# Kernel tuning notes

Measured on AMD Instinct MI355X. Metric: run time of the kernel, lower is better.

The kernel has to match this reference:

```python
import jax, jax.numpy as jnp
import numpy as np

E, K, D, H = 8, 2, 1024, 2048   # num_experts, top_k, dim, ffn_dim
B, S = 1, 1024                   # batch, seq


def setup_inputs() -> dict:
    key = jax.random.key(0)
    k0, k1, k2, k3, k4 = jax.random.split(key, 5)
    sD = 1.0 / np.sqrt(D)
    sH = 1.0 / np.sqrt(H)
    return {
        "hidden_states": jax.random.normal(k0, (B, S, D), jnp.float32),
        "gate_w": jax.random.normal(k1, (E, D), jnp.float32) * sD,
        "w1": jax.random.normal(k2, (E, D, H), jnp.float32) * sD,
        "w2": jax.random.normal(k3, (E, H, D), jnp.float32) * sH,
        "w3": jax.random.normal(k4, (E, D, H), jnp.float32) * sD,
    }


def _grouped_swiglu(x_sorted, counts, w1, w2, w3):
    """Grouped expert SwiGLU over tokens sorted by expert id.

    x_sorted: [T, D] tokens grouped contiguously by expert (expert 0 first).
    counts:   [E] number of tokens per expert (sums to T).
    """
    if hasattr(jax.lax, "ragged_dot"):
        gs = counts.astype(jnp.int32)
        h = jax.nn.silu(jax.lax.ragged_dot(x_sorted, w1, gs)) * jax.lax.ragged_dot(x_sorted, w3, gs)
        return jax.lax.ragged_dot(h, w2, gs)
    # Fallback: per-expert masked GEMM (same math; zeros pass through silu*mul).
    pos = jnp.arange(x_sorted.shape[0])
    eid = jnp.searchsorted(jnp.cumsum(counts), pos, side="right")  # expert of each sorted token
    out = jnp.zeros((x_sorted.shape[0], w2.shape[-1]), x_sorted.dtype)
    for e in range(w1.shape[0]):
        xm = jnp.where((eid == e)[:, None], x_sorted, 0.0)
        he = jax.nn.silu(xm @ w1[e]) * (xm @ w3[e])
        out = out + he @ w2[e]
    return out


def reference(hidden_states, gate_w, w1, w2, w3):
    x = hidden_states.reshape(-1, D)                      # [N, D]
    N = x.shape[0]
    # --- router: softmax over experts, then top-k ---
    scores = jax.nn.softmax(x @ gate_w.T, axis=-1)        # [N, E]
    top_scores, sel = jax.lax.top_k(scores, K)            # [N, K]
    # flatten slot-major so flat_idx % N == token id (matches `% num_tokens`)
    sel_flat = sel.T.reshape(-1)                          # [K*N]
    scores_flat = top_scores.T.reshape(-1)                # [K*N]
    # --- reorder: stable sort by expert id ---
    order = jnp.argsort(sel_flat, stable=True)            # [K*N]
    tok_sorted = order % N                                # original token per routed slot
    scores_sorted = scores_flat[order]
    counts = jnp.bincount(sel_flat, length=E)             # tokens per expert
    # --- dispatch (ep_size=1: all-to-all is identity) + grouped expert GEMM ---
    x_sorted = x[tok_sorted]                              # [K*N, D]
    y = _grouped_swiglu(x_sorted, counts, w1, w2, w3)     # [K*N, D]
    # --- weighted scatter-combine ---
    weighted = y * scores_sorted[:, None]
    out = jnp.zeros((N, D), x.dtype).at[tok_sorted].add(weighted)
    return out.reshape(hidden_states.shape)
```

## Files before the change

### kernel.cpp

```cpp
#include <hip/hip_runtime.h>
#include <hip/hip_bf16.h>
#include <math.h>

#define NE 8
#define DD 1024
#define HH 2048
#define NTOK 1024
#define NSLOT 2048
#define NSLOTP 3072

typedef short short8v __attribute__((ext_vector_type(8)));
typedef float f32x4 __attribute__((ext_vector_type(4)));

static __device__ __forceinline__ unsigned short f2bf(float f) {
  union { __hip_bfloat16 h; unsigned short u; } c;
  c.h = __float2bfloat16(f);
  return c.u;
}

static __device__ __forceinline__ short8v pk8(const float* q) {
  short8v v;
#pragma unroll
  for (int i = 0; i < 8; ++i) v[i] = (short)f2bf(q[i]);
  return v;
}

static __device__ __forceinline__ void barrier_lds() {
  asm volatile("s_waitcnt lgkmcnt(0)" ::: "memory");
  __builtin_amdgcn_s_barrier();
  asm volatile("" ::: "memory");
}

__global__ __launch_bounds__(64) void krouter(const float* __restrict__ x,
                                              const float* __restrict__ gw,
                                              int* __restrict__ e_sel,
                                              float* __restrict__ w_sel) {
  int n = blockIdx.x;
  int lane = threadIdx.x;
  const float4* xr = (const float4*)(x + (size_t)n * DD);
  const float4* gr = (const float4*)gw;
  float acc[NE];
#pragma unroll
  for (int e = 0; e < NE; ++e) acc[e] = 0.f;
#pragma unroll
  for (int i = 0; i < 4; ++i) {
    float4 xv = xr[lane + i * 64];
#pragma unroll
    for (int e = 0; e < NE; ++e) {
      float4 gv = gr[e * 256 + lane + i * 64];
      acc[e] += xv.x * gv.x + xv.y * gv.y + xv.z * gv.z + xv.w * gv.w;
    }
  }
#pragma unroll
  for (int e = 0; e < NE; ++e)
#pragma unroll
    for (int off = 32; off > 0; off >>= 1) acc[e] += __shfl_xor(acc[e], off);
  if (lane == 0) {
    float m = acc[0];
#pragma unroll
    for (int e = 1; e < NE; ++e) m = fmaxf(m, acc[e]);
    float p[NE];
    float z = 0.f;
#pragma unroll
    for (int e = 0; e < NE; ++e) { p[e] = expf(acc[e] - m); z += p[e]; }
    float inv = 1.f / z;
    int e1 = 0;
#pragma unroll
    for (int e = 1; e < NE; ++e) if (acc[e] > acc[e1]) e1 = e;
    int e2 = (e1 == 0) ? 1 : 0;
#pragma unroll
    for (int e = 0; e < NE; ++e) if (e != e1 && acc[e] > acc[e2]) e2 = e;
    e_sel[n] = e1;         w_sel[n] = p[e1] * inv;
    e_sel[NTOK + n] = e2;  w_sel[NTOK + n] = p[e2] * inv;
  }
}

__global__ __launch_bounds__(256) void kbuild(const int* __restrict__ e_sel,
                                              const float* __restrict__ w_sel,
                                              int* __restrict__ tok,
                                              float* __restrict__ wgt,
                                              int* __restrict__ meta) {
  __shared__ int sc[NE], scur[NE];
  int t = threadIdx.x;
  if (t < NE) sc[t] = 0;
  __syncthreads();
  for (int s = t; s < NSLOTP; s += 256) tok[s] = -1;
  for (int s = t; s < NSLOT; s += 256) atomicAdd(&sc[e_sel[s]], 1);
  __syncthreads();
  if (t == 0) {
    int run = 0, i64 = 0, i128 = 0;
    for (int e = 0; e < NE; ++e) {
      meta[8 + e] = run; scur[e] = run;
      meta[e] = sc[e];
      int nm = (sc[e] + 127) >> 7;
      for (int m = 0; m < nm; ++m) {
        meta[128 + i128] = e; meta[152 + i128] = m; ++i128;
      }
      for (int m = 0; m < 2 * nm; ++m) {
        meta[32 + i64] = e; meta[80 + i64] = m; ++i64;
      }
      run += nm << 7;
    }
    meta[16] = i64; meta[17] = i128;
  }
  __syncthreads();
  for (int s = t; s < NSLOT; s += 256) {
    int e = e_sel[s];
    int pos = atomicAdd(&scur[e], 1);
    tok[pos] = s & (NTOK - 1);
    wgt[pos] = w_sel[s];
  }
}

__global__ __launch_bounds__(256) void kgather(const float* __restrict__ x,
                                               const int* __restrict__ tok,
                                               unsigned short* __restrict__ xg) {
  int tid = threadIdx.x;
  int row = blockIdx.x * 2 + (tid >> 7);
  int g = tid & 127;
  int t = tok[row];
  char* dst = (char*)xg + (size_t)row * 2048 + (g << 4);
  short8v v = {0, 0, 0, 0, 0, 0, 0, 0};
  if (t >= 0) {
    const float* src = x + (size_t)t * DD + g * 8;
    float q[8];
#pragma unroll
    for (int i = 0; i < 8; ++i) q[i] = src[i];
    v = pk8(q);
  }
  *(short8v*)dst = v;
}

__global__ __launch_bounds__(256, 2) void kgemm13(
    const unsigned short* __restrict__ xg, const float* __restrict__ w1,
    const float* __restrict__ w3, unsigned short* __restrict__ hws,
    const int* __restrict__ meta) {
  __shared__ __align__(16) char smem[32768];
  char* ldsA = smem;
  char* ldsB = smem + 16384;
  int vt = blockIdx.y;
  if (vt >= meta[17]) return;
  int e = meta[128 + vt], mt = meta[152 + vt];
  int n0 = blockIdx.x * 64;
  int abase = meta[8 + e] + mt * 128;
  int tid = threadIdx.x, l = tid & 63, w = tid >> 6;
  int wm = w & 1, wn = w >> 1;

  int arow = tid >> 2, ag = tid & 3;
  const char* paA = (const char*)xg + (size_t)(abase + arow) * 2048 + (ag << 4);
  int wbA = arow * 64 + (((ag ^ (arow >> 1)) & 3) << 4);
  int bn = tid & 63, kb = tid >> 6;
  const float* pb1 = w1 + (size_t)e * DD * HH + (size_t)(kb * 8) * HH + n0 + bn;
  const float* pb3 = w3 + (size_t)e * DD * HH + (size_t)(kb * 8) * HH + n0 + bn;
  int wbB = bn * 64 + (((kb ^ (bn >> 1)) & 3) << 4);

  int afo[4];
#pragma unroll
  for (int mf = 0; mf < 4; ++mf) {
    int r = wm * 64 + mf * 16 + (l & 15);
    afo[mf] = r * 64 + ((((l >> 4) ^ (r >> 1)) & 3) << 4);
  }
  int bfo[2];
#pragma unroll
  for (int nf = 0; nf < 2; ++nf) {
    int n = wn * 32 + nf * 16 + (l & 15);
    bfo[nf] = n * 64 + ((((l >> 4) ^ (n >> 1)) & 3) << 4);
  }

  f32x4 accg[4][2], accu[4][2];
#pragma unroll
  for (int i = 0; i < 4; ++i)
#pragma unroll
    for (int j = 0; j < 2; ++j) {
      accg[i][j] = (f32x4){0.f, 0.f, 0.f, 0.f};
      accu[i][j] = (f32x4){0.f, 0.f, 0.f, 0.f};
    }

  float q1A[8], q3A[8], q1B[8], q3B[8];
  short8v aqA[2], aqB[2];
  aqA[0] = *(const short8v*)(paA);
  aqA[1] = *(const short8v*)(paA + 131072);
#pragma unroll
  for (int j = 0; j < 8; ++j) {
    q1A[j] = pb1[(size_t)j * HH];
    q3A[j] = pb3[(size_t)j * HH];
  }
  *(short8v*)(ldsA + wbA) = aqA[0];
  *(short8v*)(ldsA + 4096 + wbA) = aqA[1];
  *(short8v*)(ldsB + wbB) = pk8(q1A);
  *(short8v*)(ldsB + 4096 + wbB) = pk8(q3A);
  aqB[0] = *(const short8v*)(paA + 64);
  aqB[1] = *(const short8v*)(paA + 131072 + 64);
#pragma unroll
  for (int j = 0; j < 8; ++j) {
    q1B[j] = pb1[(size_t)(32 + j) * HH];
    q3B[j] = pb3[(size_t)(32 + j) * HH];
  }
  barrier_lds();

#define STEP13(S, QW1, QW3, AQW, QN1, QN3, AQN)                                \
  {                                                                            \
    int bo = ((S) & 1) * 8192;                                                 \
    short8v af[4], b1f[2], b3f[2];                                             \
    _Pragma("unroll") for (int mf = 0; mf < 4; ++mf)                           \
        af[mf] = *(const short8v*)(ldsA + bo + afo[mf]);                       \
    _Pragma("unroll") for (int nf = 0; nf < 2; ++nf) {                         \
      b1f[nf] = *(const short8v*)(ldsB + bo + bfo[nf]);                        \
      b3f[nf] = *(const short8v*)(ldsB + bo + 4096 + bfo[nf]);                 \
    }                                                                          \
    if ((S) < 31) {                                                            \
      int wo = (((S) + 1) & 1) * 8192;                                         \
      *(short8v*)(ldsA + wo + wbA) = AQW[0];                                   \
      *(short8v*)(ldsA + wo + 4096 + wbA) = AQW[1];                            \
      *(short8v*)(ldsB + wo + wbB) = pk8(QW1);                                 \
      *(short8v*)(ldsB + wo + 4096 + wbB) = pk8(QW3);                          \
    }                                                                          \
    if ((S) < 30) {                                                            \
      AQN[0] = *(const short8v*)(paA + ((S) + 2) * 64);                        \
      AQN[1] = *(const short8v*)(paA + 131072 + ((S) + 2) * 64);               \
      size_t ko = (size_t)((S) + 2) * 32 * HH;                                 \
      _Pragma("unroll") for (int j = 0; j < 8; ++j) {                          \
        QN1[j] = pb1[ko + (size_t)j * HH];                                     \
        QN3[j] = pb3[ko + (size_t)j * HH];                                     \
      }                                                                        \
    }                                                                          \
    _Pragma("unroll") for (int nf = 0; nf < 2; ++nf)                           \
        _Pragma("unroll") for (int mf = 0; mf < 4; ++mf) {                     \
      accg[mf][nf] = __builtin_amdgcn_mfma_f32_16x16x32_bf16(                  \
          af[mf], b1f[nf], accg[mf][nf], 0, 0, 0);                             \
      accu[mf][nf] = __builtin_amdgcn_mfma_f32_16x16x32_bf16(                  \
          af[mf], b3f[nf], accu[mf][nf], 0, 0, 0);                             \
    }                                                                          \
    if ((S) < 31) barrier_lds();                                               \
  }

  for (int ss = 0; ss < 16; ++ss) {
    int s0 = 2 * ss;
    STEP13(s0, q1B, q3B, aqB, q1A, q3A, aqA);
    STEP13(s0 + 1, q1A, q3A, aqA, q1B, q3B, aqB);
  }
#undef STEP13

  __syncthreads();
  unsigned short* hl = (unsigned short*)smem;
#pragma unroll
  for (int mf = 0; mf < 4; ++mf)
#pragma unroll
    for (int nf = 0; nf < 2; ++nf)
#pragma unroll
      for (int rr = 0; rr < 4; ++rr) {
        int row = wm * 64 + mf * 16 + ((l >> 4) << 2) + rr;
        int col = wn * 32 + nf * 16 + (l & 15);
        float gv = accg[mf][nf][rr], uv = accu[mf][nf][rr];
        hl[row * 64 + col] = f2bf((gv / (1.f + __expf(-gv))) * uv);
      }
  __syncthreads();
#pragma unroll
  for (int p = 0; p < 4; ++p) {
    int idx = p * 256 + tid;
    int row = idx >> 3, g = idx & 7;
    int dp = abase + row;
    *(short8v*)((char*)hws + (size_t)dp * 4096 + (size_t)n0 * 2 + (g << 4)) =
        *(const short8v*)((const char*)hl + row * 128 + (g << 4));
  }
}

__global__ __launch_bounds__(256, 3) void kgemm2(
    const unsigned short* __restrict__ hws, const float* __restrict__ w2,
    float* __restrict__ out, const int* __restrict__ tok,
    const float* __restrict__ wgt, const int* __restrict__ meta) {
  __shared__ __align__(16) char smem[24576];
  char* ldsA = smem;
  char* ldsB = smem + 16384;
  int vt = blockIdx.y;
  if (vt >= meta[17]) return;
  int e = meta[128 + vt], mt = meta[152 + vt];
  int n0 = blockIdx.x * 64;
  int kz = blockIdx.z;
  int mbase = meta[8 + e] + mt * 128;
  int rem = meta[e] - mt * 128;
  int tid = threadIdx.x, l = tid & 63, w = tid >> 6;
  int wm = w & 1, wn = w >> 1;

  int arow = tid >> 2, ag = tid & 3;
  const char* paA = (const char*)hws + (size_t)(mbase + arow) * 4096 +
                    kz * 2048 + (ag << 4);
  int wbA = arow * 64 + (((ag ^ (arow >> 1)) & 3) << 4);
  int bn = tid & 63, kb = tid >> 6;
  const float* pb = w2 + (size_t)e * HH * DD +
                    (size_t)(kz * 1024 + kb * 8) * DD + n0 + bn;
  int wbB = bn * 64 + (((kb ^ (bn >> 1)) & 3) << 4);

  int afo[4];
#pragma unroll
  for (int mf = 0; mf < 4; ++mf) {
    int r = wm * 64 + mf * 16 + (l & 15);
    afo[mf] = r * 64 + ((((l >> 4) ^ (r >> 1)) & 3) << 4);
  }
  int bfo[2];
#pragma unroll
  for (int nf = 0; nf < 2; ++nf) {
    int n = wn * 32 + nf * 16 + (l & 15);
    bfo[nf] = n * 64 + ((((l >> 4) ^ (n >> 1)) & 3) << 4);
  }

  f32x4 acc[4][2];
#pragma unroll
  for (int i = 0; i < 4; ++i)
#pragma unroll
    for (int j = 0; j < 2; ++j) acc[i][j] = (f32x4){0.f, 0.f, 0.f, 0.f};

  float qA[8], qB[8];
  short8v aqA[2], aqB[2];
  aqA[0] = *(const short8v*)(paA);
  aqA[1] = *(const short8v*)(paA + 262144);
#pragma unroll
  for (int j = 0; j < 8; ++j) qA[j] = pb[(size_t)j * DD];
  *(short8v*)(ldsA + wbA) = aqA[0];
  *(short8v*)(ldsA + 4096 + wbA) = aqA[1];
  *(short8v*)(ldsB + wbB) = pk8(qA);
  aqB[0] = *(const short8v*)(paA + 64);
  aqB[1] = *(const short8v*)(paA + 262144 + 64);
#pragma unroll
  for (int j = 0; j < 8; ++j) qB[j] = pb[(size_t)(32 + j) * DD];
  barrier_lds();

#define STEP2(S, QW, AQW, QN, AQN)                                             \
  {                                                                            \
    int bo = ((S) & 1) * 8192;                                                 \
    int bob = ((S) & 1) * 4096;                                                \
    short8v af[4], bf[2];                                                      \
    _Pragma("unroll") for (int mf = 0; mf < 4; ++mf)                           \
        af[mf] = *(const short8v*)(ldsA + bo + afo[mf]);                       \
    _Pragma("unroll") for (int nf = 0; nf < 2; ++nf)                           \
        bf[nf] = *(const short8v*)(ldsB + bob + bfo[nf]);                      \
    if ((S) < 31) {                                                            \
      int wo = (((S) + 1) & 1) * 8192;                                         \
      int wob = (((S) + 1) & 1) * 4096;                                        \
      *(short8v*)(ldsA + wo + wbA) = AQW[0];                                   \
      *(short8v*)(ldsA + wo + 4096 + wbA) = AQW[1];                            \
      *(short8v*)(ldsB + wob + wbB) = pk8(QW);                                 \
    }                                                                          \
    if ((S) < 30) {                                                            \
      AQN[0] = *(const short8v*)(paA + ((S) + 2) * 64);                        \
      AQN[1] = *(const short8v*)(paA + 262144 + ((S) + 2) * 64);               \
      size_t ko = (size_t)((S) + 2) * 32 * DD;                                 \
      _Pragma("unroll") for (int j = 0; j < 8; ++j)                            \
          QN[j] = pb[ko + (size_t)j * DD];                                     \
    }                                                                          \
    _Pragma("unroll") for (int nf = 0; nf < 2; ++nf)                           \
        _Pragma("unroll") for (int mf = 0; mf < 4; ++mf)                       \
            acc[mf][nf] = __builtin_amdgcn_mfma_f32_16x16x32_bf16(             \
                af[mf], bf[nf], acc[mf][nf], 0, 0, 0);                         \
    if ((S) < 31) barrier_lds();                                               \
  }

  for (int ss = 0; ss < 16; ++ss) {
    int s0 = 2 * ss;
    STEP2(s0, qB, aqB, qA, aqA);
    STEP2(s0 + 1, qA, aqA, qB, aqB);
  }
#undef STEP2

#pragma unroll
  for (int mf = 0; mf < 4; ++mf)
#pragma unroll
    for (int rr = 0; rr < 4; ++rr) {
      int row = wm * 64 + mf * 16 + ((l >> 4) << 2) + rr;
      if (row < rem) {
        int t = tok[mbase + row];
        float wt = wgt[mbase + row];
#pragma unroll
        for (int nf = 0; nf < 2; ++nf)
          atomicAdd(out + (size_t)t * DD + n0 + wn * 32 + nf * 16 + (l & 15),
                    wt * acc[mf][nf][rr]);
      }
    }
}

extern "C" void kernel_launch(void* const* d_in, const int* in_sizes, int n_in,
                              void* d_out, int out_size, void* d_ws, size_t ws_size,
                              hipStream_t stream) {
  const float* x  = (const float*)d_in[0];
  const float* gw = (const float*)d_in[1];
  const float* w1 = (const float*)d_in[2];
  const float* w2 = (const float*)d_in[3];
  const float* w3 = (const float*)d_in[4];
  float* out = (float*)d_out;
  char* ws = (char*)d_ws;
  const size_t MB = 1024 * 1024;
  if (ws_size < 24 * MB) return;

  unsigned short* xg  = (unsigned short*)(ws);
  unsigned short* hws = (unsigned short*)(ws + 6 * MB);
  char* mb = ws + 20 * MB;
  int*   e_sel  = (int*)mb;
  float* w_sel  = (float*)(mb + 8192);
  int*   tok    = (int*)(mb + 16384);
  float* wgt    = (float*)(mb + 16384 + 12288);
  int*   meta   = (int*)(mb + 16384 + 24576);

  hipMemsetAsync(out, 0, (size_t)out_size * sizeof(float), stream);
  krouter<<<dim3(NTOK), 64, 0, stream>>>(x, gw, e_sel, w_sel);
  kbuild<<<1, 256, 0, stream>>>(e_sel, w_sel, tok, wgt, meta);
  kgather<<<dim3(NSLOTP / 2), 256, 0, stream>>>(x, tok, xg);
  kgemm13<<<dim3(32, 24), 256, 0, stream>>>(xg, w1, w3, hws, meta);
  kgemm2<<<dim3(16, 24, 2), 256, 0, stream>>>(hws, w2, out, tok, wgt, meta);
}
```

Before: 108.7 us.

## Load A fragments directly from global to registers and double K-step to 64

The gate/up GEMM kernel no longer stages the bf16 activation tile through LDS. Each lane now loads its MFMA A-fragments straight from global memory into registers, double-buffered across steps. The K step per iteration grows from 32 to 64, which halves the number of barriers and iterations and uses a wider 128-byte-row swizzle for the B (weight) tile. This removes the LDS write/read traffic for A and half the synchronization, at the cost of more registers and A tiles that are no longer shared through LDS across the waves that reuse them.

Measured after the change: 130.0 us. 19.5% more time.

```diff
diff --git a/kernel.cpp b/kernel.cpp
--- a/kernel.cpp
+++ b/kernel.cpp
@@ -136,8 +136,7 @@
     const float* __restrict__ w3, unsigned short* __restrict__ hws,
     const int* __restrict__ meta) {
   __shared__ __align__(16) char smem[32768];
-  char* ldsA = smem;
-  char* ldsB = smem + 16384;
+  char* ldsB = smem;
   int vt = blockIdx.y;
   if (vt >= meta[17]) return;
   int e = meta[128 + vt], mt = meta[152 + vt];
@@ -146,26 +145,27 @@
   int tid = threadIdx.x, l = tid & 63, w = tid >> 6;
   int wm = w & 1, wn = w >> 1;
 
-  int arow = tid >> 2, ag = tid & 3;
-  const char* paA = (const char*)xg + (size_t)(abase + arow) * 2048 + (ag << 4);
-  int wbA = arow * 64 + (((ag ^ (arow >> 1)) & 3) << 4);
   int bn = tid & 63, kb = tid >> 6;
   const float* pb1 = w1 + (size_t)e * DD * HH + (size_t)(kb * 8) * HH + n0 + bn;
   const float* pb3 = w3 + (size_t)e * DD * HH + (size_t)(kb * 8) * HH + n0 + bn;
-  int wbB = bn * 64 + (((kb ^ (bn >> 1)) & 3) << 4);
-
-  int afo[4];
+  int wb1 = bn * 128 + (((kb ^ ((bn >> 1) & 7)) & 7) << 4);
+  int wb2 = bn * 128 + ((((kb + 4) ^ ((bn >> 1) & 7)) & 7) << 4);
+
+  const char* pa[4];
 #pragma unroll
   for (int mf = 0; mf < 4; ++mf) {
     int r = wm * 64 + mf * 16 + (l & 15);
-    afo[mf] = r * 64 + ((((l >> 4) ^ (r >> 1)) & 3) << 4);
-  }
-  int bfo[2];
-#pragma unroll
-  for (int nf = 0; nf < 2; ++nf) {
-    int n = wn * 32 + nf * 16 + (l & 15);
-    bfo[nf] = n * 64 + ((((l >> 4) ^ (n >> 1)) & 3) << 4);
-  }
+    pa[mf] = (const char*)xg + (size_t)(abase + r) * 2048 + ((l >> 4) << 4);
+  }
+  int bfo[2][2];
+#pragma unroll
+  for (int ks = 0; ks < 2; ++ks)
+#pragma unroll
+    for (int nf = 0; nf < 2; ++nf) {
+      int n = wn * 32 + nf * 16 + (l & 15);
+      int g = ks * 4 + (l >> 4);
+      bfo[ks][nf] = n * 128 + (((g ^ ((n >> 1) & 7)) & 7) << 4);
+    }
 
   f32x4 accg[4][2], accu[4][2];
 #pragma unroll
@@ -176,68 +176,78 @@
       accu[i][j] = (f32x4){0.f, 0.f, 0.f, 0.f};
     }
 
-  float q1A[8], q3A[8], q1B[8], q3B[8];
-  short8v aqA[2], aqB[2];
-  aqA[0] = *(const short8v*)(paA);
-  aqA[1] = *(const short8v*)(paA + 131072);
+  float q1A[16], q3A[16], q1B[16], q3B[16];
+  short8v aA[8], aB[8];
+#pragma unroll
+  for (int mf = 0; mf < 4; ++mf)
+#pragma unroll
+    for (int ks = 0; ks < 2; ++ks)
+      aA[mf * 2 + ks] = *(const short8v*)(pa[mf] + ks * 64);
 #pragma unroll
   for (int j = 0; j < 8; ++j) {
-    q1A[j] = pb1[(size_t)j * HH];
-    q3A[j] = pb3[(size_t)j * HH];
-  }
-  *(short8v*)(ldsA + wbA) = aqA[0];
-  *(short8v*)(ldsA + 4096 + wbA) = aqA[1];
-  *(short8v*)(ldsB + wbB) = pk8(q1A);
-  *(short8v*)(ldsB + 4096 + wbB) = pk8(q3A);
-  aqB[0] = *(const short8v*)(paA + 64);
-  aqB[1] = *(const short8v*)(paA + 131072 + 64);
-#pragma unroll
-  for (int j = 0; j < 8; ++j) {
-    q1B[j] = pb1[(size_t)(32 + j) * HH];
-    q3B[j] = pb3[(size_t)(32 + j) * HH];
+    q1A[j] = pb1[(size_t)j * HH];        q1A[8 + j] = pb1[(size_t)(32 + j) * HH];
+    q3A[j] = pb3[(size_t)j * HH];        q3A[8 + j] = pb3[(size_t)(32 + j) * HH];
+  }
+  *(short8v*)(ldsB + wb1) = pk8(q1A);
+  *(short8v*)(ldsB + wb2) = pk8(q1A + 8);
+  *(short8v*)(ldsB + 8192 + wb1) = pk8(q3A);
+  *(short8v*)(ldsB + 8192 + wb2) = pk8(q3A + 8);
+  {
+    size_t ko = (size_t)64 * HH;
+#pragma unroll
+    for (int j = 0; j < 8; ++j) {
+      q1B[j] = pb1[ko + (size_t)j * HH];  q1B[8 + j] = pb1[ko + (size_t)(32 + j) * HH];
+      q3B[j] = pb3[ko + (size_t)j * HH];  q3B[8 + j] = pb3[ko + (size_t)(32 + j) * HH];
+    }
   }
   barrier_lds();
 
-#define STEP13(S, QW1, QW3, AQW, QN1, QN3, AQN)                                \
+#define STEP13(S, QW1, QW3, QN1, QN3, AC, AN)                                  \
   {                                                                            \
-    int bo = ((S) & 1) * 8192;                                                 \
-    short8v af[4], b1f[2], b3f[2];                                             \
-    _Pragma("unroll") for (int mf = 0; mf < 4; ++mf)                           \
-        af[mf] = *(const short8v*)(ldsA + bo + afo[mf]);                       \
-    _Pragma("unroll") for (int nf = 0; nf < 2; ++nf) {                         \
-      b1f[nf] = *(const short8v*)(ldsB + bo + bfo[nf]);                        \
-      b3f[nf] = *(const short8v*)(ldsB + bo + 4096 + bfo[nf]);                 \
-    }                                                                          \
-    if ((S) < 31) {                                                            \
-      int wo = (((S) + 1) & 1) * 8192;                                         \
-      *(short8v*)(ldsA + wo + wbA) = AQW[0];                                   \
-      *(short8v*)(ldsA + wo + 4096 + wbA) = AQW[1];                            \
-      *(short8v*)(ldsB + wo + wbB) = pk8(QW1);                                 \
-      *(short8v*)(ldsB + wo + 4096 + wbB) = pk8(QW3);                          \
-    }                                                                          \
-    if ((S) < 30) {                                                            \
-      AQN[0] = *(const short8v*)(paA + ((S) + 2) * 64);                        \
-      AQN[1] = *(const short8v*)(paA + 131072 + ((S) + 2) * 64);               \
-      size_t ko = (size_t)((S) + 2) * 32 * HH;                                 \
+    int bo = ((S) & 1) * 16384;                                                \
+    short8v b1f[2][2], b3f[2][2];                                              \
+    _Pragma("unroll") for (int ks = 0; ks < 2; ++ks)                           \
+        _Pragma("unroll") for (int nf = 0; nf < 2; ++nf) {                     \
+      b1f[ks][nf] = *(const short8v*)(ldsB + bo + bfo[ks][nf]);                \
+      b3f[ks][nf] = *(const short8v*)(ldsB + bo + 8192 + bfo[ks][nf]);         \
+    }                                                                          \
+    if ((S) < 15) {                                                            \
+      int wo = (((S) + 1) & 1) * 16384;                                        \
+      *(short8v*)(ldsB + wo + wb1) = pk8(QW1);                                 \
+      *(short8v*)(ldsB + wo + wb2) = pk8(QW1 + 8);                             \
+      *(short8v*)(ldsB + wo + 8192 + wb1) = pk8(QW3);                          \
+      *(short8v*)(ldsB + wo + 8192 + wb2) = pk8(QW3 + 8);                      \
+    }                                                                          \
+    if ((S) < 14) {                                                            \
+      size_t ko = (size_t)((S) + 2) * 64 * HH;                                 \
       _Pragma("unroll") for (int j = 0; j < 8; ++j) {                          \
         QN1[j] = pb1[ko + (size_t)j * HH];                                     \
+        QN1[8 + j] = pb1[ko + (size_t)(32 + j) * HH];                          \
         QN3[j] = pb3[ko + (size_t)j * HH];                                     \
+        QN3[8 + j] = pb3[ko + (size_t)(32 + j) * HH];                          \
       }                                                                        \
     }                                                                          \
-    _Pragma("unroll") for (int nf = 0; nf < 2; ++nf)                           \
-        _Pragma("unroll") for (int mf = 0; mf < 4; ++mf) {                     \
+    if ((S) < 15) {                                                            \
+      _Pragma("unroll") for (int mf = 0; mf < 4; ++mf)                         \
+          _Pragma("unroll") for (int ks = 0; ks < 2; ++ks)                     \
+              AN[mf * 2 + ks] =                                                \
+                  *(const short8v*)(pa[mf] + ((S) + 1) * 128 + ks * 64);       \
+    }                                                                          \
+    _Pragma("unroll") for (int ks = 0; ks < 2; ++ks)                           \
+        _Pragma("unroll") for (int nf = 0; nf < 2; ++nf)                       \
+            _Pragma("unroll") for (int mf = 0; mf < 4; ++mf) {                 \
       accg[mf][nf] = __builtin_amdgcn_mfma_f32_16x16x32_bf16(                  \
-          af[mf], b1f[nf], accg[mf][nf], 0, 0, 0);                             \
+          AC[mf * 2 + ks], b1f[ks][nf], accg[mf][nf], 0, 0, 0);                \
       accu[mf][nf] = __builtin_amdgcn_mfma_f32_16x16x32_bf16(                  \
-          af[mf], b3f[nf], accu[mf][nf], 0, 0, 0);                             \
-    }                                                                          \
-    if ((S) < 31) barrier_lds();                                               \
-  }
-
-  for (int ss = 0; ss < 16; ++ss) {
+          AC[mf * 2 + ks], b3f[ks][nf], accu[mf][nf], 0, 0, 0);                \
+    }                                                                          \
+    if ((S) < 15) barrier_lds();                                               \
+  }
+
+  for (int ss = 0; ss < 8; ++ss) {
     int s0 = 2 * ss;
-    STEP13(s0, q1B, q3B, aqB, q1A, q3A, aqA);
-    STEP13(s0 + 1, q1A, q3A, aqA, q1B, q3B, aqB);
+    STEP13(s0, q1B, q3B, q1A, q3A, aA, aB);
+    STEP13(s0 + 1, q1A, q3A, q1B, q3B, aB, aA);
   }
 #undef STEP13
 
```

## Split fused gate/up GEMM into two kernels with SwiGLU in second epilogue

Applied to the files above, without the earlier changes.

The fused W1/W3 grouped GEMM is split into two kernels. The first computes the gate projection and stores it as bf16 in a new workspace buffer. The second computes the up projection and applies SiLU(gate)*up in its epilogue. Each kernel holds half the accumulators and half the LDS, so occupancy can rise from 2 to 3 blocks per CU. The cost is an extra launch, the A tile being read twice, an extra bf16 round-trip of the gate activations through global memory, and gate values rounded to bf16 before SiLU.

Result: slower. 122.9 us (+13.0%).

```diff
diff --git a/kernel.cpp b/kernel.cpp
--- a/kernel.cpp
+++ b/kernel.cpp
@@ -16,6 +16,12 @@
   union { __hip_bfloat16 h; unsigned short u; } c;
   c.h = __float2bfloat16(f);
   return c.u;
+}
+
+static __device__ __forceinline__ float bf2f(unsigned short u) {
+  union { unsigned int i; float f; } c;
+  c.i = (unsigned)u << 16;
+  return c.f;
 }
 
 static __device__ __forceinline__ short8v pk8(const float* q) {
@@ -131,11 +137,10 @@
   *(short8v*)dst = v;
 }
 
-__global__ __launch_bounds__(256, 2) void kgemm13(
+__global__ __launch_bounds__(256, 3) void kgemmG(
     const unsigned short* __restrict__ xg, const float* __restrict__ w1,
-    const float* __restrict__ w3, unsigned short* __restrict__ hws,
-    const int* __restrict__ meta) {
-  __shared__ __align__(16) char smem[32768];
+    unsigned short* __restrict__ g_ws, const int* __restrict__ meta) {
+  __shared__ __align__(16) char smem[24576];
   char* ldsA = smem;
   char* ldsB = smem + 16384;
   int vt = blockIdx.y;
@@ -150,8 +155,7 @@
   const char* paA = (const char*)xg + (size_t)(abase + arow) * 2048 + (ag << 4);
   int wbA = arow * 64 + (((ag ^ (arow >> 1)) & 3) << 4);
   int bn = tid & 63, kb = tid >> 6;
-  const float* pb1 = w1 + (size_t)e * DD * HH + (size_t)(kb * 8) * HH + n0 + bn;
-  const float* pb3 = w3 + (size_t)e * DD * HH + (size_t)(kb * 8) * HH + n0 + bn;
+  const float* pb = w1 + (size_t)e * DD * HH + (size_t)(kb * 8) * HH + n0 + bn;
   int wbB = bn * 64 + (((kb ^ (bn >> 1)) & 3) << 4);
 
   int afo[4];
@@ -167,79 +171,63 @@
     bfo[nf] = n * 64 + ((((l >> 4) ^ (n >> 1)) & 3) << 4);
   }
 
-  f32x4 accg[4][2], accu[4][2];
+  f32x4 acc[4][2];
 #pragma unroll
   for (int i = 0; i < 4; ++i)
 #pragma unroll
-    for (int j = 0; j < 2; ++j) {
-      accg[i][j] = (f32x4){0.f, 0.f, 0.f, 0.f};
-      accu[i][j] = (f32x4){0.f, 0.f, 0.f, 0.f};
-    }
-
-  float q1A[8], q3A[8], q1B[8], q3B[8];
+    for (int j = 0; j < 2; ++j) acc[i][j] = (f32x4){0.f, 0.f, 0.f, 0.f};
+
+  float qA[8], qB[8];
   short8v aqA[2], aqB[2];
   aqA[0] = *(const short8v*)(paA);
   aqA[1] = *(const short8v*)(paA + 131072);
 #pragma unroll
-  for (int j = 0; j < 8; ++j) {
-    q1A[j] = pb1[(size_t)j * HH];
-    q3A[j] = pb3[(size_t)j * HH];
-  }
+  for (int j = 0; j < 8; ++j) qA[j] = pb[(size_t)j * HH];
   *(short8v*)(ldsA + wbA) = aqA[0];
   *(short8v*)(ldsA + 4096 + wbA) = aqA[1];
-  *(short8v*)(ldsB + wbB) = pk8(q1A);
-  *(short8v*)(ldsB + 4096 + wbB) = pk8(q3A);
+  *(short8v*)(ldsB + wbB) = pk8(qA);
   aqB[0] = *(const short8v*)(paA + 64);
   aqB[1] = *(const short8v*)(paA + 131072 + 64);
 #pragma unroll
-  for (int j = 0; j < 8; ++j) {
-    q1B[j] = pb1[(size_t)(32 + j) * HH];
-    q3B[j] = pb3[(size_t)(32 + j) * HH];
-  }
+  for (int j = 0; j < 8; ++j) qB[j] = pb[(size_t)(32 + j) * HH];
   barrier_lds();
 
-#define STEP13(S, QW1, QW3, AQW, QN1, QN3, AQN)                                \
+#define STEPG(S, QW, AQW, QN, AQN)                                             \
   {                                                                            \
     int bo = ((S) & 1) * 8192;                                                 \
-    short8v af[4], b1f[2], b3f[2];                                             \
+    int bob = ((S) & 1) * 4096;                                                \
+    short8v af[4], bf[2];                                                      \
     _Pragma("unroll") for (int mf = 0; mf < 4; ++mf)                           \
         af[mf] = *(const short8v*)(ldsA + bo + afo[mf]);                       \
-    _Pragma("unroll") for (int nf = 0; nf < 2; ++nf) {                         \
-      b1f[nf] = *(const short8v*)(ldsB + bo + bfo[nf]);                        \
-      b3f[nf] = *(const short8v*)(ldsB + bo + 4096 + bfo[nf]);                 \
-    }                                                                          \
+    _Pragma("unroll") for (int nf = 0; nf < 2; ++nf)                           \
+        bf[nf] = *(const short8v*)(ldsB + bob + bfo[nf]);                      \
     if ((S) < 31) {                                                            \
       int wo = (((S) + 1) & 1) * 8192;                                         \
+      int wob = (((S) + 1) & 1) * 4096;                                        \
       *(short8v*)(ldsA + wo + wbA) = AQW[0];                                   \
       *(short8v*)(ldsA + wo + 4096 + wbA) = AQW[1];                            \
-      *(short8v*)(ldsB + wo + wbB) = pk8(QW1);                                 \
-      *(short8v*)(ldsB + wo + 4096 + wbB) = pk8(QW3);                          \
+      *(short8v*)(ldsB + wob + wbB) = pk8(QW);                                 \
     }                                                                          \
     if ((S) < 30) {                                                            \
       AQN[0] = *(const short8v*)(paA + ((S) + 2) * 64);                        \
       AQN[1] = *(const short8v*)(paA + 131072 + ((S) + 2) * 64);               \
       size_t ko = (size_t)((S) + 2) * 32 * HH;                                 \
-      _Pragma("unroll") for (int j = 0; j < 8; ++j) {                          \
-        QN1[j] = pb1[ko + (size_t)j * HH];                                     \
-        QN3[j] = pb3[ko + (size_t)j * HH];                                     \
-      }                                                                        \
+      _Pragma("unroll") for (int j = 0; j < 8; ++j)                            \
+          QN[j] = pb[ko + (size_t)j * HH];                                     \
     }                                                                          \
     _Pragma("unroll") for (int nf = 0; nf < 2; ++nf)                           \
-        _Pragma("unroll") for (int mf = 0; mf < 4; ++mf) {                     \
-      accg[mf][nf] = __builtin_amdgcn_mfma_f32_16x16x32_bf16(                  \
-          af[mf], b1f[nf], accg[mf][nf], 0, 0, 0);                             \
-      accu[mf][nf] = __builtin_amdgcn_mfma_f32_16x16x32_bf16(                  \
-          af[mf], b3f[nf], accu[mf][nf], 0, 0, 0);                             \
-    }                                                                          \
+        _Pragma("unroll") for (int mf = 0; mf < 4; ++mf)                       \
+            acc[mf][nf] = __builtin_amdgcn_mfma_f32_16x16x32_bf16(             \
+                af[mf], bf[nf], acc[mf][nf], 0, 0, 0);                         \
     if ((S) < 31) barrier_lds();                                               \
   }
 
   for (int ss = 0; ss < 16; ++ss) {
     int s0 = 2 * ss;
-    STEP13(s0, q1B, q3B, aqB, q1A, q3A, aqA);
-    STEP13(s0 + 1, q1A, q3A, aqA, q1B, q3B, aqB);
-  }
-#undef STEP13
+    STEPG(s0, qB, aqB, qA, aqA);
+    STEPG(s0 + 1, qA, aqA, qB, aqB);
+  }
+#undef STEPG
 
   __syncthreads();
   unsigned short* hl = (unsigned short*)smem;
@@ -251,8 +239,7 @@
       for (int rr = 0; rr < 4; ++rr) {
         int row = wm * 64 + mf * 16 + ((l >> 4) << 2) + rr;
         int col = wn * 32 + nf * 16 + (l & 15);
-        float gv = accg[mf][nf][rr], uv = accu[mf][nf][rr];
-        hl[row * 64 + col] = f2bf((gv / (1.f + __expf(-gv))) * uv);
+        hl[row * 64 + col] = f2bf(acc[mf][nf][rr]);
       }
   __syncthreads();
 #pragma unroll
@@ -260,8 +247,133 @@
     int idx = p * 256 + tid;
     int row = idx >> 3, g = idx & 7;
     int dp = abase + row;
-    *(short8v*)((char*)hws + (size_t)dp * 4096 + (size_t)n0 * 2 + (g << 4)) =
+    *(short8v*)((char*)g_ws + (size_t)dp * 4096 + (size_t)n0 * 2 + (g << 4)) =
         *(const short8v*)((const char*)hl + row * 128 + (g << 4));
+  }
+}
+
+__global__ __launch_bounds__(256, 3) void kgemmU(
+    const unsigned short* __restrict__ xg, const float* __restrict__ w3,
+    const unsigned short* __restrict__ g_ws, unsigned short* __restrict__ hws,
+    const int* __restrict__ meta) {
+  __shared__ __align__(16) char smem[24576];
+  char* ldsA = smem;
+  char* ldsB = smem + 16384;
+  int vt = blockIdx.y;
+  if (vt >= meta[17]) return;
+  int e = meta[128 + vt], mt = meta[152 + vt];
+  int n0 = blockIdx.x * 64;
+  int abase = meta[8 + e] + mt * 128;
+  int tid = threadIdx.x, l = tid & 63, w = tid >> 6;
+  int wm = w & 1, wn = w >> 1;
+
+  int arow = tid >> 2, ag = tid & 3;
+  const char* paA = (const char*)xg + (size_t)(abase + arow) * 2048 + (ag << 4);
+  int wbA = arow * 64 + (((ag ^ (arow >> 1)) & 3) << 4);
+  int bn = tid & 63, kb = tid >> 6;
+  const float* pb = w3 + (size_t)e * DD * HH + (size_t)(kb * 8) * HH + n0 + bn;
+  int wbB = bn * 64 + (((kb ^ (bn >> 1)) & 3) << 4);
+
+  int afo[4];
+#pragma unroll
+  for (int mf = 0; mf < 4; ++mf) {
+    int r = wm * 64 + mf * 16 + (l & 15);
+    afo[mf] = r * 64 + ((((l >> 4) ^ (r >> 1)) & 3) << 4);
+  }
+  int bfo[2];
+#pragma unroll
+  for (int nf = 0; nf < 2; ++nf) {
+    int n = wn * 32 + nf * 16 + (l & 15);
+    bfo[nf] = n * 64 + ((((l >> 4) ^ (n >> 1)) & 3) << 4);
+  }
+
+  f32x4 acc[4][2];
+#pragma unroll
+  for (int i = 0; i < 4; ++i)
+#pragma unroll
+    for (int j = 0; j < 2; ++j) acc[i][j] = (f32x4){0.f, 0.f, 0.f, 0.f};
+
+  float qA[8], qB[8];
+  short8v aqA[2], aqB[2];
+  aqA[0] = *(const short8v*)(paA);
+  aqA[1] = *(const short8v*)(paA + 131072);
+#pragma unroll
+  for (int j = 0; j < 8; ++j) qA[j] = pb[(size_t)j * HH];
+  *(short8v*)(ldsA + wbA) = aqA[0];
+  *(short8v*)(ldsA + 4096 + wbA) = aqA[1];
+  *(short8v*)(ldsB + wbB) = pk8(qA);
+  aqB[0] = *(const short8v*)(paA + 64);
+  aqB[1] = *(const short8v*)(paA + 131072 + 64);
+#pragma unroll
+  for (int j = 0; j < 8; ++j) qB[j] = pb[(size_t)(32 + j) * HH];
+  barrier_lds();
+
+#define STEPU(S, QW, AQW, QN, AQN)                                             \
+  {                                                                            \
+    int bo = ((S) & 1) * 8192;                                                 \
+    int bob = ((S) & 1) * 4096;                                                \
+    short8v af[4], bf[2];                                                      \
+    _Pragma("unroll") for (int mf = 0; mf < 4; ++mf)                           \
+        af[mf] = *(const short8v*)(ldsA + bo + afo[mf]);                       \
+    _Pragma("unroll") for (int nf = 0; nf < 2; ++nf)                           \
+        bf[nf] = *(const short8v*)(ldsB + bob + bfo[nf]);                      \
+    if ((S) < 31) {                                                            \
+      int wo = (((S) + 1) & 1) * 8192;                                         \
+      int wob = (((S) + 1) & 1) * 4096;                                        \
+      *(short8v*)(ldsA + wo + wbA) = AQW[0];                                   \
+      *(short8v*)(ldsA + wo + 4096 + wbA) = AQW[1];                            \
+      *(short8v*)(ldsB + wob + wbB) = pk8(QW);                                 \
+    }                                                                          \
+    if ((S) < 30) {                                                            \
+      AQN[0] = *(const short8v*)(paA + ((S) + 2) * 64);                        \
+      AQN[1] = *(const short8v*)(paA + 131072 + ((S) + 2) * 64);               \
+      size_t ko = (size_t)((S) + 2) * 32 * HH;                                 \
+      _Pragma("unroll") for (int j = 0; j < 8; ++j)                            \
+          QN[j] = pb[ko + (size_t)j * HH];                                     \
+    }                                                                          \
+    _Pragma("unroll") for (int nf = 0; nf < 2; ++nf)                           \
+        _Pragma("unroll") for (int mf = 0; mf < 4; ++mf)                       \
+            acc[mf][nf] = __builtin_amdgcn_mfma_f32_16x16x32_bf16(             \
+                af[mf], bf[nf], acc[mf][nf], 0, 0, 0);                         \
+    if ((S) < 31) barrier_lds();                                               \
+  }
+
+  for (int ss = 0; ss < 16; ++ss) {
+    int s0 = 2 * ss;
+    STEPU(s0, qB, aqB, qA, aqA);
+    STEPU(s0 + 1, qA, aqA, qB, aqB);
+  }
+#undef STEPU
+
+  __syncthreads();
+  unsigned short* hl = (unsigned short*)smem;
+#pragma unroll
+  for (int mf = 0; mf < 4; ++mf)
+#pragma unroll
+    for (int nf = 0; nf < 2; ++nf)
+#pragma unroll
+      for (int rr = 0; rr < 4; ++rr) {
+        int row = wm * 64 + mf * 16 + ((l >> 4) << 2) + rr;
+        int col = wn * 32 + nf * 16 + (l & 15);
+        hl[row * 64 + col] = f2bf(acc[mf][nf][rr]);
+      }
+  __syncthreads();
+#pragma unroll
+  for (int p = 0; p < 4; ++p) {
+    int idx = p * 256 + tid;
+    int row = idx >> 3, g = idx & 7;
+    int dp = abase + row;
+    size_t off = (size_t)dp * 4096 + (size_t)n0 * 2 + (g << 4);
+    short8v u8 = *(const short8v*)((const char*)hl + row * 128 + (g << 4));
+    short8v g8 = *(const short8v*)((const char*)g_ws + off);
+    short8v h8;
+#pragma unroll
+    for (int i = 0; i < 8; ++i) {
+      float gv = bf2f((unsigned short)g8[i]);
+      float uv = bf2f((unsigned short)u8[i]);
+      h8[i] = (short)f2bf((gv / (1.f + __expf(-gv))) * uv);
+    }
+    *(short8v*)((char*)hws + off) = h8;
   }
 }
 
@@ -389,11 +501,12 @@
   float* out = (float*)d_out;
   char* ws = (char*)d_ws;
   const size_t MB = 1024 * 1024;
-  if (ws_size < 24 * MB) return;
-
-  unsigned short* xg  = (unsigned short*)(ws);
-  unsigned short* hws = (unsigned short*)(ws + 6 * MB);
-  char* mb = ws + 20 * MB;
+  if (ws_size < 32 * MB) return;
+
+  unsigned short* xg   = (unsigned short*)(ws);
+  unsigned short* hws  = (unsigned short*)(ws + 6 * MB);
+  unsigned short* g_ws = (unsigned short*)(ws + 18 * MB);
+  char* mb = ws + 30 * MB;
   int*   e_sel  = (int*)mb;
   float* w_sel  = (float*)(mb + 8192);
   int*   tok    = (int*)(mb + 16384);
@@ -404,6 +517,7 @@
   krouter<<<dim3(NTOK), 64, 0, stream>>>(x, gw, e_sel, w_sel);
   kbuild<<<1, 256, 0, stream>>>(e_sel, w_sel, tok, wgt, meta);
   kgather<<<dim3(NSLOTP / 2), 256, 0, stream>>>(x, tok, xg);
-  kgemm13<<<dim3(32, 24), 256, 0, stream>>>(xg, w1, w3, hws, meta);
+  kgemmG<<<dim3(32, 24), 256, 0, stream>>>(xg, w1, g_ws, meta);
+  kgemmU<<<dim3(32, 24), 256, 0, stream>>>(xg, w3, g_ws, hws, meta);
   kgemm2<<<dim3(16, 24, 2), 256, 0, stream>>>(hws, w2, out, tok, wgt, meta);
 }
```
